# Kernel tuning notes

Measured on AMD Instinct MI355X. Metric: run time of the kernel, lower is better.

## Reference

```python
import jax, jax.numpy as jnp
import numpy as np

N_IMG = 1024
N_VIEWS = 90


def _bilinear(img, yi, xi):
    """Bilinear sample img at float coords (yi=row, xi=col); 0 outside (skimage warp cval=0)."""
    n = img.shape[0]
    y0 = jnp.floor(yi)
    x0 = jnp.floor(xi)
    wy = yi - y0
    wx = xi - x0
    y0i = y0.astype(jnp.int32)
    x0i = x0.astype(jnp.int32)

    def get(yy, xx):
        valid = (yy >= 0) & (yy < n) & (xx >= 0) & (xx < n)
        v = img[jnp.clip(yy, 0, n - 1), jnp.clip(xx, 0, n - 1)]
        return jnp.where(valid, v, jnp.zeros((), img.dtype))

    v00 = get(y0i, x0i)
    v01 = get(y0i, x0i + 1)
    v10 = get(y0i + 1, x0i)
    v11 = get(y0i + 1, x0i + 1)
    return (v00 * (1 - wy) * (1 - wx) + v01 * (1 - wy) * wx
            + v10 * wy * (1 - wx) + v11 * wy * wx)


def radon_jax(image, theta_deg):
    """skimage.transform.radon(image, theta, circle=True) equivalent.
    Rotate image by each angle (bilinear, about center = N//2, inverse map as in
    skimage warp) and sum over rows. Returns sinogram [N, n_angles]."""
    n = image.shape[0]
    center = n // 2
    ang = jnp.deg2rad(theta_deg.astype(image.dtype))
    cos_a = jnp.cos(ang)  # [A]
    sin_a = jnp.sin(ang)
    coords = jnp.arange(n, dtype=image.dtype)
    X, Y = jnp.meshgrid(coords, coords)  # X = col (x), Y = row (y), [N, N]

    def rotate_and_sum(ca, sa):
        # inverse map: src = R @ dst (homogeneous, (x, y) order) as in skimage radon
        x_in = ca * X + sa * Y - center * (ca + sa - 1)
        y_in = -sa * X + ca * Y - center * (ca - sa - 1)
        rotated = _bilinear(image, y_in, x_in)  # [N, N]
        return rotated.sum(axis=0)  # sum over rows -> projection [N]

    sino = jax.vmap(rotate_and_sum)(cos_a, sin_a)  # [A, N]
    return sino.T  # [N, A] to match skimage radon layout


def setup_inputs() -> dict:
    key = jax.random.key(0)
    k1, _ = jax.random.split(key)
    x = jax.random.normal(k1, (N_IMG, N_IMG), dtype=jnp.float32)
    theta = jnp.arange(N_VIEWS, dtype=jnp.float32) * 2.0  # 0..178 deg, 2-deg spacing
    return {"x": x, "theta": theta}


def reference(x, theta):
    return radon_jax(x, theta)
```

## Files before the change

kernel.cpp:

```cpp
#include <hip/hip_runtime.h>

#define N_IMG   1024
#define N_VIEWS 90
#define CENTER  512
#define TILE    64
#define NYB     (N_IMG / TILE)
#define NTHREADS 512
#define NWAVES   8
#define YPT      (TILE / NWAVES)
#define TILE_WORDS 9216

__device__ __forceinline__ void map_coords(float ca, float sa, float cx, float cy,
                                           float Xf, float Yf,
                                           float& x_in, float& y_in) {
    const float fx0 = fmaf(ca, Xf, cx);
    const float fy0 = fmaf(-sa, Xf, cy);
    x_in = fmaf(sa, Yf, fx0);
    y_in = fmaf(ca, Yf, fy0);
}

__device__ __forceinline__ void gload_lds4(const float* g, float* l) {
    __builtin_amdgcn_global_load_lds((const __attribute__((address_space(1))) void*)g,
                                     (__attribute__((address_space(3))) void*)l,
                                     4, 0, 0);
}
__device__ __forceinline__ void gload_lds16(const float* g, float* l) {
    __builtin_amdgcn_global_load_lds((const __attribute__((address_space(1))) void*)g,
                                     (__attribute__((address_space(3))) void*)l,
                                     16, 0, 0);
}

template<int STRIDE>
__device__ __forceinline__ float sample_tile(const float* __restrict__ tile,
                                             float sa, float ca,
                                             float x_in, float y_in,
                                             float basef, int iy0, int win,
                                             bool interior) {
    float acc = 0.0f;
    const float Sf = (float)STRIDE;
    if (interior) {
        #pragma unroll
        for (int i = 0; i < YPT; ++i) {
            const float x0f = floorf(x_in);
            const float y0f = floorf(y_in);
            const float wx  = x_in - x0f;
            const float wy  = y_in - y0f;
            const int li = (int)(fmaf(y0f, Sf, x0f) + basef);
            const float t00 = tile[li];
            const float t01 = tile[li + 1];
            const float t10 = tile[li + STRIDE];
            const float t11 = tile[li + STRIDE + 1];
            const float top = fmaf(wx, t01 - t00, t00);
            const float bot = fmaf(wx, t11 - t10, t10);
            acc += fmaf(wy, bot - top, top);
            x_in += sa; y_in += ca;
        }
    } else {
        #pragma unroll
        for (int i = 0; i < YPT; ++i) {
            const float x0f = floorf(x_in);
            const float y0f = floorf(y_in);
            const float wx  = x_in - x0f;
            const float wy  = y_in - y0f;
            const int x0 = (int)x0f;
            const int y0 = (int)y0f;
            const int x0c = min(max(x0,     0), N_IMG - 1);
            const int x1c = min(max(x0 + 1, 0), N_IMG - 1);
            const int y0c = min(max(y0,     0), N_IMG - 1);
            const int y1c = min(max(y0 + 1, 0), N_IMG - 1);
            const float wxa = (x0     >= 0 && x0     < N_IMG) ? (1.0f - wx) : 0.0f;
            const float wxb = (x0 + 1 >= 0 && x0 + 1 < N_IMG) ? wx          : 0.0f;
            const float wya = (y0     >= 0 && y0     < N_IMG) ? (1.0f - wy) : 0.0f;
            const float wyb = (y0 + 1 >= 0 && y0 + 1 < N_IMG) ? wy          : 0.0f;
            const int r0 = (y0c - iy0) * STRIDE - win;
            const int r1 = (y1c - iy0) * STRIDE - win;
            const float t00 = tile[r0 + x0c];
            const float t01 = tile[r0 + x1c];
            const float t10 = tile[r1 + x0c];
            const float t11 = tile[r1 + x1c];
            acc += wya * fmaf(wxa, t00, wxb * t01)
                 + wyb * fmaf(wxa, t10, wxb * t11);
            x_in += sa; y_in += ca;
        }
    }
    return acc;
}

__global__ __launch_bounds__(NTHREADS) void radon_tile(const float* __restrict__ img,
                                                       const float* __restrict__ theta,
                                                       float* __restrict__ partial,
                                                       float* __restrict__ out,
                                                       int mode) {
    __shared__ float tile[TILE_WORDS];
    __shared__ float fpar[4];
    __shared__ int   ipar[7];

    const int a  = blockIdx.z;
    const int X0 = blockIdx.x * TILE;
    const int Y0 = blockIdx.y * TILE;
    const int tid  = threadIdx.x;
    const int lane = tid & 63;
    const int wv   = tid >> 6;

    if (wv == 0) {
        const float ang = theta[a] * 0.017453292519943295f;
        float sa, ca;
        __sincosf(ang, &sa, &ca);
        const float cx = (float)CENTER * (1.0f - ca - sa);
        const float cy = (float)CENTER * (1.0f - ca + sa);

        float x00, y00, x01, y01, x10, y10, x11, y11;
        map_coords(ca, sa, cx, cy, (float)X0,        (float)Y0,        x00, y00);
        map_coords(ca, sa, cx, cy, (float)(X0 + 63), (float)Y0,        x01, y01);
        map_coords(ca, sa, cx, cy, (float)X0,        (float)(Y0 + 63), x10, y10);
        map_coords(ca, sa, cx, cy, (float)(X0 + 63), (float)(Y0 + 63), x11, y11);
        const float xmin = fminf(fminf(x00, x01), fminf(x10, x11));
        const float xmax = fmaxf(fmaxf(x00, x01), fmaxf(x10, x11));
        const float ymin = fminf(fminf(y00, y01), fminf(y10, y11));
        const float ymax = fmaxf(fmaxf(y00, y01), fmaxf(y10, y11));

        const int ix0_raw = (int)floorf(xmin);
        const int ix1_raw = (int)floorf(xmax) + 1;
        const int iy0_raw = (int)floorf(ymin);
        const int iy1_raw = (int)floorf(ymax) + 1;

        const int ix0 = max(0, ix0_raw);
        const int ix1 = min(N_IMG - 1, ix1_raw);
        const int iy0 = max(0, iy0_raw);
        const int iy1 = min(N_IMG - 1, iy1_raw);

        int path, win, dB = 0;
        if (fabsf(ca) > 0.7072f) {
            path = 0; win = min(ix0 & ~3, N_IMG - 96);
        } else {
            path = (ca > 0.0f) ? 1 : 2;
            win = min(ix0, N_IMG - 64);
            dB  = max(win, ix1 - 63) - win;
        }
        if (tid == 0) {
            fpar[0] = sa; fpar[1] = ca; fpar[2] = cx; fpar[3] = cy;
            ipar[0] = iy0; ipar[1] = iy1 - iy0 + 1; ipar[2] = win; ipar[3] = dB;
            ipar[4] = path;
            ipar[5] = (ix0_raw >= 0) && (ix1_raw <= N_IMG - 1) &&
                      (iy0_raw >= 0) && (iy1_raw <= N_IMG - 1);
            ipar[6] = (ix1 < ix0) || (iy1 < iy0);
        }
    }
    __syncthreads();

    float* __restrict__ pslot = partial + ((size_t)(a * NYB + blockIdx.y) << 10) + X0;

    if (ipar[6]) {
        if (mode == 0 && tid < 64) pslot[tid] = 0.0f;
        return;
    }

    const float sa = fpar[0], ca = fpar[1], cx = fpar[2], cy = fpar[3];
    const int iy0 = ipar[0], h = ipar[1], win = ipar[2], dB = ipar[3];
    const int path = ipar[4];
    const bool interior = ipar[5];

    const int X = X0 + lane;
    const float Xf  = (float)X;
    const float fx0 = fmaf(ca, Xf, cx);
    const float fy0 = fmaf(-sa, Xf, cy);
    const float Ybf = (float)(Y0 + wv * YPT);
    const float x_in = fmaf(sa, Ybf, fx0);
    const float y_in = fmaf(ca, Ybf, fy0);

    float acc;
    if (path == 0) {
        const int D = h * 96;
        for (int o = wv * 256; o < D; o += NWAVES * 256) {
            const int d = o + 4 * lane;
            const int r = (unsigned)d / 96u;
            const int c = d - r * 96;
            const int gr = min(iy0 + r, N_IMG - 1);
            gload_lds16(img + (size_t)gr * N_IMG + win + c, tile + o);
        }
        __syncthreads();
        acc = sample_tile<96>(tile, sa, ca, x_in, y_in,
                              -(float)(iy0 * 96 + win), iy0, win, interior);
    } else {
        const int STRIDE = (path == 1) ? 95 : 97;
        {
            const float* g = img + (size_t)(iy0 + wv) * N_IMG + win + lane;
            float* l = tile + wv * STRIDE;
            for (int r = wv; r < h; r += NWAVES) {
                gload_lds4(g, l);
                if (dB > 0) gload_lds4(g + dB, l + dB);
                g += NWAVES * N_IMG;
                l += NWAVES * STRIDE;
            }
        }
        __syncthreads();
        if (path == 1)
            acc = sample_tile<95>(tile, sa, ca, x_in, y_in,
                                  -(float)(iy0 * 95 + win), iy0, win, interior);
        else
            acc = sample_tile<97>(tile, sa, ca, x_in, y_in,
                                  -(float)(iy0 * 97 + win), iy0, win, interior);
    }

    __syncthreads();
    tile[wv * 64 + lane] = acc;
    __syncthreads();
    if (wv == 0) {
        float s = 0.0f;
        #pragma unroll
        for (int w = 0; w < NWAVES; ++w) s += tile[w * 64 + lane];
        if (mode == 0) pslot[lane] = s;
        else           atomicAdd(&out[X * N_VIEWS + a], s);
    }
}

__global__ __launch_bounds__(256) void reduce_partials(const float* __restrict__ partial,
                                                       float* __restrict__ out) {
    const int g = blockIdx.x * 256 + threadIdx.x;
    const int a = g >> 10;
    const int X = g & 1023;
    float s = 0.0f;
    #pragma unroll
    for (int yb = 0; yb < NYB; ++yb)
        s += partial[((size_t)(a * NYB + yb) << 10) + X];
    out[X * N_VIEWS + a] = s;
}

extern "C" void kernel_launch(void* const* d_in, const int* in_sizes, int n_in,
                              void* d_out, int out_size, void* d_ws, size_t ws_size,
                              hipStream_t stream) {
    const float* img   = (const float*)d_in[0];
    const float* theta = (const float*)d_in[1];
    float* out     = (float*)d_out;
    float* partial = (float*)d_ws;

    const size_t needed = (size_t)N_VIEWS * NYB * N_IMG * sizeof(float);
    const int mode = (ws_size >= needed) ? 0 : 1;
    if (mode == 1)
        hipMemsetAsync(d_out, 0, (size_t)out_size * sizeof(float), stream);

    dim3 grid(N_IMG / TILE, N_IMG / TILE, N_VIEWS);
    radon_tile<<<grid, NTHREADS, 0, stream>>>(img, theta, partial, out, mode);

    if (mode == 0)
        reduce_partials<<<(N_VIEWS * N_IMG) / 256, 256, 0, stream>>>(partial, out);
}
```

Baseline: 144.4 us.

## Loop over Y tiles per block with double-buffered LDS staging, drop partials reduction

```diff
diff --git a/kernel.cpp b/kernel.cpp
--- a/kernel.cpp
+++ b/kernel.cpp
@@ -4,11 +4,13 @@
 #define N_VIEWS 90
 #define CENTER  512
 #define TILE    64
-#define NYB     (N_IMG / TILE)
+#define NTILES  16
 #define NTHREADS 512
 #define NWAVES   8
 #define YPT      (TILE / NWAVES)
-#define TILE_WORDS 9216
+#define BUF_WORDS 9216
+
+extern __shared__ float smem[];
 
 __device__ __forceinline__ void map_coords(float ca, float sa, float cx, float cy,
                                            float Xf, float Yf,
@@ -21,13 +23,70 @@
 
 __device__ __forceinline__ void gload_lds4(const float* g, float* l) {
     __builtin_amdgcn_global_load_lds((const __attribute__((address_space(1))) void*)g,
-                                     (__attribute__((address_space(3))) void*)l,
-                                     4, 0, 0);
+                                     (__attribute__((address_space(3))) void*)l, 4, 0, 0);
 }
 __device__ __forceinline__ void gload_lds16(const float* g, float* l) {
     __builtin_amdgcn_global_load_lds((const __attribute__((address_space(1))) void*)g,
-                                     (__attribute__((address_space(3))) void*)l,
-                                     16, 0, 0);
+                                     (__attribute__((address_space(3))) void*)l, 16, 0, 0);
+}
+
+__device__ __forceinline__ void compute_params(int* dst, float X0f, float Y0f,
+                                               float sa, float ca, float cx, float cy,
+                                               bool wide, bool store) {
+    float x00, y00, x01, y01, x10, y10, x11, y11;
+    map_coords(ca, sa, cx, cy, X0f,         Y0f,         x00, y00);
+    map_coords(ca, sa, cx, cy, X0f + 63.f,  Y0f,         x01, y01);
+    map_coords(ca, sa, cx, cy, X0f,         Y0f + 63.f,  x10, y10);
+    map_coords(ca, sa, cx, cy, X0f + 63.f,  Y0f + 63.f,  x11, y11);
+    const float xmin = fminf(fminf(x00, x01), fminf(x10, x11));
+    const float xmax = fmaxf(fmaxf(x00, x01), fmaxf(x10, x11));
+    const float ymin = fminf(fminf(y00, y01), fminf(y10, y11));
+    const float ymax = fmaxf(fmaxf(y00, y01), fmaxf(y10, y11));
+    const int ix0_raw = (int)floorf(xmin);
+    const int ix1_raw = (int)floorf(xmax) + 1;
+    const int iy0_raw = (int)floorf(ymin);
+    const int iy1_raw = (int)floorf(ymax) + 1;
+    const int ix0 = max(0, ix0_raw), ix1 = min(N_IMG - 1, ix1_raw);
+    const int iy0 = max(0, iy0_raw), iy1 = min(N_IMG - 1, iy1_raw);
+    int win, dB = 0;
+    if (wide) {
+        win = min(ix0 & ~3, N_IMG - 96);
+    } else {
+        win = min(ix0, N_IMG - 64);
+        dB  = max(win, ix1 - 63) - win;
+    }
+    int flags = ((ix1 < ix0) || (iy1 < iy0)) ? 1 : 0;
+    flags |= ((ix0_raw >= 0) && (ix1_raw <= N_IMG - 1) &&
+              (iy0_raw >= 0) && (iy1_raw <= N_IMG - 1)) ? 2 : 0;
+    if (store) {
+        dst[0] = iy0; dst[1] = iy1 - iy0 + 1; dst[2] = win; dst[3] = dB; dst[4] = flags;
+    }
+}
+
+__device__ __forceinline__ void stage_wide(const float* __restrict__ img, float* buf,
+                                           int lane, int wv, int iy0, int h, int win) {
+    const int D = h * 96;
+    for (int o = wv * 256; o < D; o += NWAVES * 256) {
+        const int d = o + 4 * lane;
+        const int r = (unsigned)d / 96u;
+        const int c = d - r * 96;
+        const int gr = min(iy0 + r, N_IMG - 1);
+        gload_lds16(img + (size_t)gr * N_IMG + win + c, buf + o);
+    }
+}
+
+template<int STRIDE>
+__device__ __forceinline__ void stage_steep(const float* __restrict__ img, float* buf,
+                                            int lane, int wv, int iy0, int h,
+                                            int win, int dB) {
+    const float* g = img + (size_t)(iy0 + wv) * N_IMG + win + lane;
+    float* l = buf + wv * STRIDE;
+    for (int r = wv; r < h; r += NWAVES) {
+        gload_lds4(g, l);
+        if (dB > 0) gload_lds4(g + dB, l + dB);
+        g += NWAVES * N_IMG;
+        l += NWAVES * STRIDE;
+    }
 }
 
 template<int STRIDE>
@@ -86,144 +145,96 @@
     return acc;
 }
 
-__global__ __launch_bounds__(NTHREADS) void radon_tile(const float* __restrict__ img,
-                                                       const float* __restrict__ theta,
-                                                       float* __restrict__ partial,
-                                                       float* __restrict__ out,
-                                                       int mode) {
-    __shared__ float tile[TILE_WORDS];
-    __shared__ float fpar[4];
-    __shared__ int   ipar[7];
-
-    const int a  = blockIdx.z;
-    const int X0 = blockIdx.x * TILE;
-    const int Y0 = blockIdx.y * TILE;
-    const int tid  = threadIdx.x;
-    const int lane = tid & 63;
-    const int wv   = tid >> 6;
-
-    if (wv == 0) {
-        const float ang = theta[a] * 0.017453292519943295f;
-        float sa, ca;
-        __sincosf(ang, &sa, &ca);
-        const float cx = (float)CENTER * (1.0f - ca - sa);
-        const float cy = (float)CENTER * (1.0f - ca + sa);
-
-        float x00, y00, x01, y01, x10, y10, x11, y11;
-        map_coords(ca, sa, cx, cy, (float)X0,        (float)Y0,        x00, y00);
-        map_coords(ca, sa, cx, cy, (float)(X0 + 63), (float)Y0,        x01, y01);
-        map_coords(ca, sa, cx, cy, (float)X0,        (float)(Y0 + 63), x10, y10);
-        map_coords(ca, sa, cx, cy, (float)(X0 + 63), (float)(Y0 + 63), x11, y11);
-        const float xmin = fminf(fminf(x00, x01), fminf(x10, x11));
-        const float xmax = fmaxf(fmaxf(x00, x01), fmaxf(x10, x11));
-        const float ymin = fminf(fminf(y00, y01), fminf(y10, y11));
-        const float ymax = fmaxf(fmaxf(y00, y01), fmaxf(y10, y11));
-
-        const int ix0_raw = (int)floorf(xmin);
-        const int ix1_raw = (int)floorf(xmax) + 1;
-        const int iy0_raw = (int)floorf(ymin);
-        const int iy1_raw = (int)floorf(ymax) + 1;
-
-        const int ix0 = max(0, ix0_raw);
-        const int ix1 = min(N_IMG - 1, ix1_raw);
-        const int iy0 = max(0, iy0_raw);
-        const int iy1 = min(N_IMG - 1, iy1_raw);
-
-        int path, win, dB = 0;
-        if (fabsf(ca) > 0.7072f) {
-            path = 0; win = min(ix0 & ~3, N_IMG - 96);
-        } else {
-            path = (ca > 0.0f) ? 1 : 2;
-            win = min(ix0, N_IMG - 64);
-            dB  = max(win, ix1 - 63) - win;
-        }
-        if (tid == 0) {
-            fpar[0] = sa; fpar[1] = ca; fpar[2] = cx; fpar[3] = cy;
-            ipar[0] = iy0; ipar[1] = iy1 - iy0 + 1; ipar[2] = win; ipar[3] = dB;
-            ipar[4] = path;
-            ipar[5] = (ix0_raw >= 0) && (ix1_raw <= N_IMG - 1) &&
-                      (iy0_raw >= 0) && (iy1_raw <= N_IMG - 1);
-            ipar[6] = (ix1 < ix0) || (iy1 < iy0);
-        }
-    }
+template<int STRIDE>
+__device__ __forceinline__ void run_pipeline(const float* __restrict__ img,
+                                             float* __restrict__ out,
+                                             int X0, int a,
+                                             float sa, float ca, float cx, float cy,
+                                             int lane, int wv, int tid,
+                                             int (*ipar)[5]) {
+    constexpr bool WIDE = (STRIDE == 96);
+    float* buf0 = smem;
+    float* buf1 = smem + BUF_WORDS;
+    const float X0f = (float)X0;
+
+    if (wv == 0)
+        compute_params(ipar[0], X0f, 0.0f, sa, ca, cx, cy, WIDE, tid == 0);
     __syncthreads();
-
-    float* __restrict__ pslot = partial + ((size_t)(a * NYB + blockIdx.y) << 10) + X0;
-
-    if (ipar[6]) {
-        if (mode == 0 && tid < 64) pslot[tid] = 0.0f;
-        return;
-    }
-
-    const float sa = fpar[0], ca = fpar[1], cx = fpar[2], cy = fpar[3];
-    const int iy0 = ipar[0], h = ipar[1], win = ipar[2], dB = ipar[3];
-    const int path = ipar[4];
-    const bool interior = ipar[5];
-
-    const int X = X0 + lane;
-    const float Xf  = (float)X;
+    {
+        const int* p = ipar[0];
+        if (!(p[4] & 1)) {
+            if (WIDE) stage_wide(img, buf0, lane, wv, p[0], p[1], p[2]);
+            else      stage_steep<STRIDE>(img, buf0, lane, wv, p[0], p[1], p[2], p[3]);
+        }
+    }
+    if (wv == 0)
+        compute_params(ipar[1], X0f, (float)TILE, sa, ca, cx, cy, WIDE, tid == 0);
+    __syncthreads();
+
+    const float Xf  = X0f + (float)lane;
     const float fx0 = fmaf(ca, Xf, cx);
     const float fy0 = fmaf(-sa, Xf, cy);
-    const float Ybf = (float)(Y0 + wv * YPT);
-    const float x_in = fmaf(sa, Ybf, fx0);
-    const float y_in = fmaf(ca, Ybf, fy0);
-
-    float acc;
-    if (path == 0) {
-        const int D = h * 96;
-        for (int o = wv * 256; o < D; o += NWAVES * 256) {
-            const int d = o + 4 * lane;
-            const int r = (unsigned)d / 96u;
-            const int c = d - r * 96;
-            const int gr = min(iy0 + r, N_IMG - 1);
-            gload_lds16(img + (size_t)gr * N_IMG + win + c, tile + o);
+
+    float acc = 0.0f;
+    for (int t = 0; t < NTILES; ++t) {
+        const int* pt = ipar[t % 3];
+        const int iy0 = pt[0], win = pt[2], fl = pt[4];
+
+        if (t + 1 < NTILES) {
+            const int* pn = ipar[(t + 1) % 3];
+            if (!(pn[4] & 1)) {
+                float* nb = ((t + 1) & 1) ? buf1 : buf0;
+                if (WIDE) stage_wide(img, nb, lane, wv, pn[0], pn[1], pn[2]);
+                else      stage_steep<STRIDE>(img, nb, lane, wv, pn[0], pn[1], pn[2], pn[3]);
+            }
+        }
+        if (wv == 0 && t + 2 < NTILES)
+            compute_params(ipar[(t + 2) % 3], X0f, (float)((t + 2) * TILE),
+                           sa, ca, cx, cy, WIDE, tid == 0);
+
+        if (!(fl & 1)) {
+            const float Ybf  = (float)(t * TILE + wv * YPT);
+            const float x_in = fmaf(sa, Ybf, fx0);
+            const float y_in = fmaf(ca, Ybf, fy0);
+            acc += sample_tile<STRIDE>((t & 1) ? buf1 : buf0, sa, ca, x_in, y_in,
+                                       -(float)(iy0 * STRIDE + win), iy0, win,
+                                       (fl & 2) != 0);
         }
         __syncthreads();
-        acc = sample_tile<96>(tile, sa, ca, x_in, y_in,
-                              -(float)(iy0 * 96 + win), iy0, win, interior);
-    } else {
-        const int STRIDE = (path == 1) ? 95 : 97;
-        {
-            const float* g = img + (size_t)(iy0 + wv) * N_IMG + win + lane;
-            float* l = tile + wv * STRIDE;
-            for (int r = wv; r < h; r += NWAVES) {
-                gload_lds4(g, l);
-                if (dB > 0) gload_lds4(g + dB, l + dB);
-                g += NWAVES * N_IMG;
-                l += NWAVES * STRIDE;
-            }
-        }
-        __syncthreads();
-        if (path == 1)
-            acc = sample_tile<95>(tile, sa, ca, x_in, y_in,
-                                  -(float)(iy0 * 95 + win), iy0, win, interior);
-        else
-            acc = sample_tile<97>(tile, sa, ca, x_in, y_in,
-                                  -(float)(iy0 * 97 + win), iy0, win, interior);
-    }
-
-    __syncthreads();
-    tile[wv * 64 + lane] = acc;
+    }
+
+    smem[wv * 64 + lane] = acc;
     __syncthreads();
     if (wv == 0) {
         float s = 0.0f;
         #pragma unroll
-        for (int w = 0; w < NWAVES; ++w) s += tile[w * 64 + lane];
-        if (mode == 0) pslot[lane] = s;
-        else           atomicAdd(&out[X * N_VIEWS + a], s);
-    }
-}
-
-__global__ __launch_bounds__(256) void reduce_partials(const float* __restrict__ partial,
+        for (int w = 0; w < NWAVES; ++w) s += smem[w * 64 + lane];
+        out[(size_t)(X0 + lane) * N_VIEWS + a] = s;
+    }
+}
+
+__global__ __launch_bounds__(NTHREADS) void radon_full(const float* __restrict__ img,
+                                                       const float* __restrict__ theta,
                                                        float* __restrict__ out) {
-    const int g = blockIdx.x * 256 + threadIdx.x;
-    const int a = g >> 10;
-    const int X = g & 1023;
-    float s = 0.0f;
-    #pragma unroll
-    for (int yb = 0; yb < NYB; ++yb)
-        s += partial[((size_t)(a * NYB + yb) << 10) + X];
-    out[X * N_VIEWS + a] = s;
+    __shared__ int ipar[3][5];
+    const int X0  = blockIdx.x * TILE;
+    const int a   = blockIdx.y;
+    const int tid = threadIdx.x;
+    const int lane = tid & 63;
+    const int wv   = tid >> 6;
+
+    const float ang = theta[a] * 0.017453292519943295f;
+    float sa, ca;
+    __sincosf(ang, &sa, &ca);
+    const float cx = (float)CENTER * (1.0f - ca - sa);
+    const float cy = (float)CENTER * (1.0f - ca + sa);
+
+    if (fabsf(ca) > 0.7072f)
+        run_pipeline<96>(img, out, X0, a, sa, ca, cx, cy, lane, wv, tid, ipar);
+    else if (ca > 0.0f)
+        run_pipeline<95>(img, out, X0, a, sa, ca, cx, cy, lane, wv, tid, ipar);
+    else
+        run_pipeline<97>(img, out, X0, a, sa, ca, cx, cy, lane, wv, tid, ipar);
 }
 
 extern "C" void kernel_launch(void* const* d_in, const int* in_sizes, int n_in,
@@ -231,17 +242,8 @@
                               hipStream_t stream) {
     const float* img   = (const float*)d_in[0];
     const float* theta = (const float*)d_in[1];
-    float* out     = (float*)d_out;
-    float* partial = (float*)d_ws;
-
-    const size_t needed = (size_t)N_VIEWS * NYB * N_IMG * sizeof(float);
-    const int mode = (ws_size >= needed) ? 0 : 1;
-    if (mode == 1)
-        hipMemsetAsync(d_out, 0, (size_t)out_size * sizeof(float), stream);
-
-    dim3 grid(N_IMG / TILE, N_IMG / TILE, N_VIEWS);
-    radon_tile<<<grid, NTHREADS, 0, stream>>>(img, theta, partial, out, mode);
-
-    if (mode == 0)
-        reduce_partials<<<(N_VIEWS * N_IMG) / 256, 256, 0, stream>>>(partial, out);
-}
+    float* out = (float*)d_out;
+
+    dim3 grid(N_IMG / TILE, N_VIEWS);
+    radon_full<<<grid, NTHREADS, 2 * BUF_WORDS * sizeof(float), stream>>>(img, theta, out);
+}
```

Measured after the change: 159.6 us. +10.6%, slower.
